# Kernel optimization log

Measured on AMD Instinct MI355X. Metric: run time of the kernel, lower is better.

Reference implementation:

```python
import jax, jax.numpy as jnp
import numpy as np

TIME_STEP = 3
TOPK = 84


def setup_inputs() -> dict:
    key = jax.random.key(0)
    kx, _ = jax.random.split(key)
    x = jax.random.uniform(kx, (8, 2, 352, 2048), dtype=jnp.float32)
    w = jnp.ones((), dtype=jnp.float32)
    return {"x": x, "w": w}


def reference(x, w):
    b, c, f, l = x.shape
    emb = c * TIME_STEP
    last = x[:, :, :, -1:]  # (b,c,f,1) last frame, used as right-padding
    # shift i: x[..., i:] padded on the right with i copies of the last frame
    parts = [
        x if i == 0 else jnp.concatenate(
            [x[:, :, :, i:], jnp.broadcast_to(last, (b, c, f, i))], axis=-1)
        for i in range(TIME_STEP)
    ]
    shifted = jnp.concatenate(parts, axis=1)            # (b, emb, f, l)
    shifted = shifted.transpose(0, 2, 3, 1).reshape(b, f * l, emb)  # (b, N, emb)

    query = shifted.mean(axis=1, keepdims=True)         # (b, 1, emb)
    scores = jnp.einsum('bqe,bne->bqn', query, shifted)[:, 0]  # (b, N)

    topk_scores, topk_idx = jax.lax.top_k(scores, TOPK)  # (b, K)
    vals = jnp.take_along_axis(shifted, topk_idx[:, :, None], axis=1)  # (b, K, emb)
    attn = jax.nn.softmax(topk_scores, axis=-1)          # (b, K)

    out = jnp.einsum('bk,bke->be', attn, vals) * w + query[:, 0] * (0.5 - w)  # (b, emb)
    return out.reshape(b, c, 1, TIME_STEP)
```

## Files before the change

kernel.cpp:

```cpp
#include <hip/hip_runtime.h>
#include <math.h>

#define LL 2048
#define FF 352
#define BATCH 8
#define TOPK 84
#define FPB 4
#define BPB (FF / FPB)
#define NBINS 8192
#define BINSCALE 1024.0f
#define SUBBINS 8192
#define CAP 32768
#define FCAP 1024
#define NROWS (BATCH * 2 * FF)
#define FL (FF * LL)
#define CNTSTRIDE 64

#define OFF_Q 64
#define OFF_CNT 128
#define OFF_PART 1024
#define OFF_CS 32768
#define OFF_CI 294912

__device__ __forceinline__ int coarse_bin(float sv) {
    int bin = (int)(fmaxf(sv, 0.f) * BINSCALE);
    return bin > NBINS - 1 ? NBINS - 1 : bin;
}
__device__ __forceinline__ int fine_bin(float sv, int t) {
    float f = fmaxf(sv, 0.f) * BINSCALE - (float)t;
    int s = (int)(f * (float)SUBBINS);
    s = s < 0 ? 0 : s;
    return s > SUBBINS - 1 ? SUBBINS - 1 : s;
}

__device__ __forceinline__ void find_thresh(const unsigned int* hist, int K,
                                            int tid, int lane, int wid,
                                            int* wtot, int* sres) {
    int csum = 0;
    #pragma unroll
    for (int k = 0; k < 32; ++k) csum += (int)hist[tid * 32 + ((k + tid) & 31)];
    int sfx = csum;
    #pragma unroll
    for (int d = 1; d < 64; d <<= 1) {
        int o = __shfl_down(sfx, d);
        if (lane + d < 64) sfx += o;
    }
    if (lane == 0) wtot[wid] = sfx;
    __syncthreads();
    int hi = 0;
    #pragma unroll
    for (int w2 = 0; w2 < 4; ++w2) if (w2 > wid) hi += wtot[w2];
    int SC = sfx + hi;
    int SCn = SC - csum;
    if (SC >= K && SCn < K) { sres[0] = tid; sres[1] = SCn; }
    __syncthreads();
    int cstar = sres[0], aboveC = sres[1];
    if (tid < 64) {
        int hv = (tid < 32) ? (int)hist[cstar * 32 + tid] : 0;
        int s2 = hv;
        #pragma unroll
        for (int d = 1; d < 32; d <<= 1) {
            int o = __shfl_down(s2, d);
            if (tid + d < 64) s2 += o;
        }
        int ge = aboveC + s2;
        int gt = ge - hv;
        if (tid < 32 && ge >= K && gt < K) { sres[2] = cstar * 32 + tid; sres[3] = gt; }
    }
    __syncthreads();
}

__global__ __launch_bounds__(256) void k_rowsum(const float* __restrict__ x,
                                                float* __restrict__ ws,
                                                int* __restrict__ wsi) {
    int r = blockIdx.x;
    int tid = threadIdx.x;
    if (r == 0 && tid < 8) wsi[OFF_CNT + tid * CNTSTRIDE] = 0;
    const float4* rp = (const float4*)(x + (size_t)r * LL);
    float4 v0 = rp[tid];
    float4 v1 = rp[tid + 256];
    float s = v0.x + v0.y + v0.z + v0.w + v1.x + v1.y + v1.z + v1.w;
    for (int off = 32; off; off >>= 1) s += __shfl_down(s, off);
    __shared__ float red[4];
    int lane = tid & 63, wid = tid >> 6;
    if (lane == 0) red[wid] = s;
    __syncthreads();
    float* part = ws + OFF_PART + 4 * r;
    if (tid == 0) {
        part[0] = red[0] + red[1] + red[2] + red[3];
        part[1] = v0.x;
        part[2] = v0.y;
    }
    if (tid == 255) part[3] = v1.w;
}

__global__ __launch_bounds__(256, 4) void k_score(const float* __restrict__ x,
                                                  float* __restrict__ ws,
                                                  int* __restrict__ wsi) {
    __shared__ unsigned int hist[NBINS];
    __shared__ float4 red0[4], red1[4];
    __shared__ float sq[6];
    __shared__ int wtot[4], sres[4];
    __shared__ int lcnt, lbase;
    int tid = threadIdx.x;
    int b = blockIdx.x / BPB, blk = blockIdx.x % BPB;
    int fb = blk * FPB;
    int lane = tid & 63, wid = tid >> 6;

    for (int k = 0; k < NBINS / 256; ++k) hist[tid + (k << 8)] = 0u;
    if (tid == 0) lcnt = 0;

    float4 acc0 = {0.f, 0.f, 0.f, 0.f}, acc1 = {0.f, 0.f, 0.f, 0.f};
    const float4* part = (const float4*)(ws + OFF_PART) + b * 2 * FF;
    for (int i = tid; i < 2 * FF; i += 256) {
        float4 p = part[i];
        if (i < FF) { acc0.x += p.x; acc0.y += p.y; acc0.z += p.z; acc0.w += p.w; }
        else        { acc1.x += p.x; acc1.y += p.y; acc1.z += p.z; acc1.w += p.w; }
    }
    for (int off = 32; off; off >>= 1) {
        acc0.x += __shfl_down(acc0.x, off); acc0.y += __shfl_down(acc0.y, off);
        acc0.z += __shfl_down(acc0.z, off); acc0.w += __shfl_down(acc0.w, off);
        acc1.x += __shfl_down(acc1.x, off); acc1.y += __shfl_down(acc1.y, off);
        acc1.z += __shfl_down(acc1.z, off); acc1.w += __shfl_down(acc1.w, off);
    }
    if (lane == 0) { red0[wid] = acc0; red1[wid] = acc1; }
    __syncthreads();
    if (tid == 0) {
        float A0 = 0, B0 = 0, C0 = 0, D0 = 0, A1 = 0, B1 = 0, C1 = 0, D1 = 0;
        for (int w2 = 0; w2 < 4; ++w2) {
            A0 += red0[w2].x; B0 += red0[w2].y; C0 += red0[w2].z; D0 += red0[w2].w;
            A1 += red1[w2].x; B1 += red1[w2].y; C1 += red1[w2].z; D1 += red1[w2].w;
        }
        const float inv = 1.f / (float)FL;
        sq[0] = A0 * inv;
        sq[1] = A1 * inv;
        sq[2] = (A0 - B0 + D0) * inv;
        sq[3] = (A1 - B1 + D1) * inv;
        sq[4] = (A0 - B0 - C0 + 2.f * D0) * inv;
        sq[5] = (A1 - B1 - C1 + 2.f * D1) * inv;
        if (blk == 0) for (int e = 0; e < 6; ++e) ws[OFF_Q + b * 6 + e] = sq[e];
    }
    __syncthreads();
    float q0 = sq[0], q1 = sq[1], q2 = sq[2], q3 = sq[3], q4 = sq[4], q5 = sq[5];

    const float* r0p[FPB];
    const float* r1p[FPB];
    #pragma unroll
    for (int fr = 0; fr < FPB; ++fr) {
        r0p[fr] = x + ((size_t)(b * 2 + 0) * FF + fb + fr) * LL;
        r1p[fr] = x + ((size_t)(b * 2 + 1) * FF + fb + fr) * LL;
    }

    float pa4[FPB][2], pa5[FPB][2], pb4[FPB][2], pb5[FPB][2];
    if (lane == 63) {
        #pragma unroll
        for (int fr = 0; fr < FPB; ++fr) {
            #pragma unroll
            for (int h = 0; h < 2; ++h) {
                int l0 = (h << 10) + tid * 4;
                if (l0 != LL - 4) {
                    pa4[fr][h] = r0p[fr][l0 + 4]; pa5[fr][h] = r0p[fr][l0 + 5];
                    pb4[fr][h] = r1p[fr][l0 + 4]; pb5[fr][h] = r1p[fr][l0 + 5];
                }
            }
        }
    }

    float4 sreg[FPB][2];
    float4 u = *(const float4*)(r0p[0] + tid * 4);
    float4 v = *(const float4*)(r1p[0] + tid * 4);
    #pragma unroll
    for (int fr = 0; fr < FPB; ++fr) {
        #pragma unroll
        for (int h = 0; h < 2; ++h) {
            int l0 = (h << 10) + tid * 4;
            int nfr = (h == 1) ? fr + 1 : fr;
            int nh = (h == 1) ? 0 : 1;
            float4 un, vn;
            bool have_next = (nfr < FPB);
            if (have_next) {
                int ln = (nh << 10) + tid * 4;
                un = *(const float4*)(r0p[nfr] + ln);
                vn = *(const float4*)(r1p[nfr] + ln);
            }
            float a4 = __shfl_down(u.x, 1), a5 = __shfl_down(u.y, 1);
            float b4 = __shfl_down(v.x, 1), b5 = __shfl_down(v.y, 1);
            if (lane == 63) {
                if (l0 == LL - 4) { a4 = u.w; a5 = u.w; b4 = v.w; b5 = v.w; }
                else { a4 = pa4[fr][h]; a5 = pa5[fr][h];
                       b4 = pb4[fr][h]; b5 = pb5[fr][h]; }
            }
            float4 s;
            s.x = q0 * u.x + q1 * v.x + q2 * u.y + q3 * v.y + q4 * u.z + q5 * v.z;
            s.y = q0 * u.y + q1 * v.y + q2 * u.z + q3 * v.z + q4 * u.w + q5 * v.w;
            s.z = q0 * u.z + q1 * v.z + q2 * u.w + q3 * v.w + q4 * a4 + q5 * b4;
            s.w = q0 * u.w + q1 * v.w + q2 * a4 + q3 * b4 + q4 * a5 + q5 * b5;
            sreg[fr][h] = s;
            #pragma unroll
            for (int j = 0; j < 4; ++j) {
                float sv = j == 0 ? s.x : (j == 1 ? s.y : (j == 2 ? s.z : s.w));
                atomicAdd(&hist[coarse_bin(sv)], 1u);
            }
            if (have_next) { u = un; v = vn; }
        }
    }
    __syncthreads();

    find_thresh(hist, TOPK, tid, lane, wid, wtot, sres);
    int t = sres[2];

    unsigned int kmask = 0u;
    #pragma unroll
    for (int fr = 0; fr < FPB; ++fr) {
        #pragma unroll
        for (int h = 0; h < 2; ++h) {
            float4 s = sreg[fr][h];
            #pragma unroll
            for (int j = 0; j < 4; ++j) {
                float sv = j == 0 ? s.x : (j == 1 ? s.y : (j == 2 ? s.z : s.w));
                if (coarse_bin(sv) >= t) kmask |= 1u << ((fr << 3) + (h << 2) + j);
            }
        }
    }
    int cnt = __popc(kmask);
    int myoff = 0;
    if (cnt) myoff = atomicAdd(&lcnt, cnt);
    __syncthreads();
    if (tid == 0) lbase = atomicAdd(&wsi[OFF_CNT + b * CNTSTRIDE], lcnt);
    __syncthreads();
    int pos = lbase + myoff;
    #pragma unroll
    for (int fr = 0; fr < FPB; ++fr) {
        #pragma unroll
        for (int h = 0; h < 2; ++h) {
            float4 s = sreg[fr][h];
            int l0 = (h << 10) + tid * 4;
            int nb = (fb + fr) * LL + l0;
            #pragma unroll
            for (int j = 0; j < 4; ++j) {
                if (kmask & (1u << ((fr << 3) + (h << 2) + j))) {
                    float sv = j == 0 ? s.x : (j == 1 ? s.y : (j == 2 ? s.z : s.w));
                    if (pos < CAP) {
                        ws[OFF_CS + b * CAP + pos] = sv;
                        wsi[OFF_CI + b * CAP + pos] = nb + j;
                    }
                    ++pos;
                }
            }
        }
    }
}

__global__ __launch_bounds__(256) void k_final(const float* __restrict__ x,
                                               const float* __restrict__ wv,
                                               const float* __restrict__ ws,
                                               const int* __restrict__ wsi,
                                               float* __restrict__ out) {
    __shared__ union {
        unsigned int hist[NBINS];
        struct { float cs[FCAP]; int ci[FCAP]; } fin;
    } sh;
    __shared__ int wtot[4], sres[4];
    __shared__ int cnt2;
    __shared__ float redm[4];
    __shared__ float den;
    __shared__ float accsh[8];
    int tid = threadIdx.x;
    int b = blockIdx.x;
    int lane = tid & 63, wid = tid >> 6;

    int C = wsi[OFF_CNT + b * CNTSTRIDE];
    if (C > CAP) C = CAP;
    const float* gcs = ws + OFF_CS + b * CAP;
    const int* gci = wsi + OFF_CI + b * CAP;

    for (int k = 0; k < NBINS / 256; ++k) sh.hist[tid + (k << 8)] = 0u;
    __syncthreads();
    for (int p4 = tid * 4; p4 < C; p4 += 1024) {
        float4 s4 = *(const float4*)(gcs + p4);
        int lim = C - p4;
        atomicAdd(&sh.hist[coarse_bin(s4.x)], 1u);
        if (lim > 1) atomicAdd(&sh.hist[coarse_bin(s4.y)], 1u);
        if (lim > 2) atomicAdd(&sh.hist[coarse_bin(s4.z)], 1u);
        if (lim > 3) atomicAdd(&sh.hist[coarse_bin(s4.w)], 1u);
    }
    __syncthreads();
    find_thresh(sh.hist, TOPK, tid, lane, wid, wtot, sres);
    int t = sres[2];
    int above = sres[3];

    for (int k = 0; k < NBINS / 256; ++k) sh.hist[tid + (k << 8)] = 0u;
    __syncthreads();
    for (int p4 = tid * 4; p4 < C; p4 += 1024) {
        float4 s4 = *(const float4*)(gcs + p4);
        int lim = C - p4;
        #pragma unroll
        for (int j = 0; j < 4; ++j) {
            if (j >= lim) break;
            float sv = j == 0 ? s4.x : (j == 1 ? s4.y : (j == 2 ? s4.z : s4.w));
            if (coarse_bin(sv) == t) atomicAdd(&sh.hist[fine_bin(sv, t)], 1u);
        }
    }
    __syncthreads();
    find_thresh(sh.hist, TOPK - above, tid, lane, wid, wtot, sres);
    int t2 = sres[2];
    if (tid == 0) cnt2 = 0;
    __syncthreads();

    for (int p4 = tid * 4; p4 < C; p4 += 1024) {
        float4 s4 = *(const float4*)(gcs + p4);
        int4 i4 = *(const int4*)(gci + p4);
        int lim = C - p4;
        #pragma unroll
        for (int j = 0; j < 4; ++j) {
            if (j >= lim) break;
            float sv = j == 0 ? s4.x : (j == 1 ? s4.y : (j == 2 ? s4.z : s4.w));
            int iv = j == 0 ? i4.x : (j == 1 ? i4.y : (j == 2 ? i4.z : i4.w));
            int bin = coarse_bin(sv);
            bool keep = (bin > t) || (bin == t && fine_bin(sv, t) >= t2);
            if (keep) {
                int q = atomicAdd(&cnt2, 1);
                if (q < FCAP) { sh.fin.cs[q] = sv; sh.fin.ci[q] = iv; }
            }
        }
    }
    __syncthreads();
    int C2 = cnt2;
    if (C2 > FCAP) C2 = FCAP;

    if (tid < 8) accsh[tid] = 0.f;
    if (tid == 0) den = 0.f;
    __syncthreads();

    float m = -INFINITY;
    for (int p = tid; p < C2; p += 256) m = fmaxf(m, sh.fin.cs[p]);
    for (int off = 32; off; off >>= 1) m = fmaxf(m, __shfl_down(m, off));
    if (lane == 0) redm[wid] = m;
    __syncthreads();
    float smax = fmaxf(fmaxf(redm[0], redm[1]), fmaxf(redm[2], redm[3]));

    float g0 = 0.f, g1 = 0.f, g2 = 0.f, g3 = 0.f, g4 = 0.f, g5 = 0.f, dden = 0.f;
    for (int p = tid; p < C2; p += 256) {
        float s = sh.fin.cs[p];
        int idx = sh.fin.ci[p];
        int rank = 0;
        for (int j = 0; j < C2; ++j) {
            float sj = sh.fin.cs[j];
            int ij = sh.fin.ci[j];
            rank += (sj > s) || (sj == s && ij < idx);
        }
        if (rank < TOPK) {
            float pexp = expf(s - smax);
            dden += pexp;
            int f = idx >> 11, l = idx & (LL - 1);
            int l1 = l + 1 < LL ? l + 1 : LL - 1;
            int l2 = l + 2 < LL ? l + 2 : LL - 1;
            const float* r0 = x + ((size_t)(b * 2 + 0) * FF + f) * LL;
            const float* r1 = x + ((size_t)(b * 2 + 1) * FF + f) * LL;
            g0 += pexp * r0[l];
            g1 += pexp * r1[l];
            g2 += pexp * r0[l1];
            g3 += pexp * r1[l1];
            g4 += pexp * r0[l2];
            g5 += pexp * r1[l2];
        }
    }
    for (int off = 32; off; off >>= 1) {
        dden += __shfl_down(dden, off);
        g0 += __shfl_down(g0, off); g1 += __shfl_down(g1, off);
        g2 += __shfl_down(g2, off); g3 += __shfl_down(g3, off);
        g4 += __shfl_down(g4, off); g5 += __shfl_down(g5, off);
    }
    if (lane == 0) {
        atomicAdd(&den, dden);
        atomicAdd(&accsh[0], g0); atomicAdd(&accsh[1], g1);
        atomicAdd(&accsh[2], g2); atomicAdd(&accsh[3], g3);
        atomicAdd(&accsh[4], g4); atomicAdd(&accsh[5], g5);
    }
    __syncthreads();
    if (tid < 6) {
        float w = wv[0];
        float q = ws[OFF_Q + b * 6 + tid];
        out[b * 6 + tid] = (accsh[tid] / den) * w + q * (0.5f - w);
    }
}

extern "C" void kernel_launch(void* const* d_in, const int* in_sizes, int n_in,
                              void* d_out, int out_size, void* d_ws, size_t ws_size,
                              hipStream_t stream) {
    const float* x = (const float*)d_in[0];
    const float* w = (const float*)d_in[1];
    float* out = (float*)d_out;
    float* wsf = (float*)d_ws;
    int* wsi = (int*)d_ws;

    k_rowsum<<<NROWS, 256, 0, stream>>>(x, wsf, wsi);
    k_score<<<BATCH * BPB, 256, 0, stream>>>(x, wsf, wsi);
    k_final<<<BATCH, 256, 0, stream>>>(x, w, wsf, wsi, out);
}
```

Baseline: 117.7 us.

## Batch rows in rowsum and compact candidates in shared memory for final select

k_rowsum now has each block reduce 8 rows and emit one partial per group of rows, which cuts the block count and the number of partials k_score must sum. k_final no longer makes three passes over the global candidate list. It makes one histogram pass, then copies candidates in or above the threshold bin into a shared buffer, and runs the fine histogram and final filter on that smaller buffer. The global reads are unrolled four float4 loads per thread. The risk is that if more than 2048 candidates fall at or above the threshold bin, the buffer truncates them, and the shared memory footprint is larger.

```diff
diff --git a/kernel.cpp b/kernel.cpp
--- a/kernel.cpp
+++ b/kernel.cpp
@@ -11,7 +11,10 @@
 #define BINSCALE 1024.0f
 #define SUBBINS 8192
 #define CAP 32768
-#define FCAP 1024
+#define BCAP 2048
+#define FINCAP 512
+#define RPB 8
+#define NPART (NROWS / RPB)
 #define NROWS (BATCH * 2 * FF)
 #define FL (FF * LL)
 #define CNTSTRIDE 64
@@ -33,12 +36,14 @@
     return s > SUBBINS - 1 ? SUBBINS - 1 : s;
 }
 
+template<int NB>
 __device__ __forceinline__ void find_thresh(const unsigned int* hist, int K,
                                             int tid, int lane, int wid,
                                             int* wtot, int* sres) {
+    constexpr int CW = NB / 256;
     int csum = 0;
     #pragma unroll
-    for (int k = 0; k < 32; ++k) csum += (int)hist[tid * 32 + ((k + tid) & 31)];
+    for (int k = 0; k < CW; ++k) csum += (int)hist[tid * CW + ((k + tid) & (CW - 1))];
     int sfx = csum;
     #pragma unroll
     for (int d = 1; d < 64; d <<= 1) {
@@ -56,16 +61,16 @@
     __syncthreads();
     int cstar = sres[0], aboveC = sres[1];
     if (tid < 64) {
-        int hv = (tid < 32) ? (int)hist[cstar * 32 + tid] : 0;
+        int hv = (tid < CW) ? (int)hist[cstar * CW + tid] : 0;
         int s2 = hv;
         #pragma unroll
-        for (int d = 1; d < 32; d <<= 1) {
+        for (int d = 1; d < CW; d <<= 1) {
             int o = __shfl_down(s2, d);
             if (tid + d < 64) s2 += o;
         }
         int ge = aboveC + s2;
         int gt = ge - hv;
-        if (tid < 32 && ge >= K && gt < K) { sres[2] = cstar * 32 + tid; sres[3] = gt; }
+        if (tid < CW && ge >= K && gt < K) { sres[2] = cstar * CW + tid; sres[3] = gt; }
     }
     __syncthreads();
 }
@@ -73,25 +78,37 @@
 __global__ __launch_bounds__(256) void k_rowsum(const float* __restrict__ x,
                                                 float* __restrict__ ws,
                                                 int* __restrict__ wsi) {
-    int r = blockIdx.x;
+    int g = blockIdx.x;
     int tid = threadIdx.x;
-    if (r == 0 && tid < 8) wsi[OFF_CNT + tid * CNTSTRIDE] = 0;
-    const float4* rp = (const float4*)(x + (size_t)r * LL);
-    float4 v0 = rp[tid];
-    float4 v1 = rp[tid + 256];
-    float s = v0.x + v0.y + v0.z + v0.w + v1.x + v1.y + v1.z + v1.w;
-    for (int off = 32; off; off >>= 1) s += __shfl_down(s, off);
-    __shared__ float red[4];
+    if (g == 0 && tid < 8) wsi[OFF_CNT + tid * CNTSTRIDE] = 0;
+    int bc = g / 44, sub = g % 44;
+    int rr = tid >> 5, c = tid & 31;
+    const float4* rp = (const float4*)(x + (size_t)(bc * FF + sub * RPB + rr) * LL);
+    float s = 0.f, x0c = 0.f, x1c = 0.f, xlc = 0.f;
+    #pragma unroll
+    for (int k = 0; k < 16; ++k) {
+        float4 v = rp[c + (k << 5)];
+        s += v.x + v.y + v.z + v.w;
+        if (k == 0 && c == 0) { x0c = v.x; x1c = v.y; }
+        if (k == 15 && c == 31) xlc = v.w;
+    }
     int lane = tid & 63, wid = tid >> 6;
-    if (lane == 0) red[wid] = s;
-    __syncthreads();
-    float* part = ws + OFF_PART + 4 * r;
+    for (int off = 32; off; off >>= 1) {
+        s += __shfl_down(s, off);
+        x0c += __shfl_down(x0c, off);
+        x1c += __shfl_down(x1c, off);
+        xlc += __shfl_down(xlc, off);
+    }
+    __shared__ float4 red[4];
+    if (lane == 0) red[wid] = make_float4(s, x0c, x1c, xlc);
+    __syncthreads();
     if (tid == 0) {
-        part[0] = red[0] + red[1] + red[2] + red[3];
-        part[1] = v0.x;
-        part[2] = v0.y;
-    }
-    if (tid == 255) part[3] = v1.w;
+        float4 p = make_float4(0.f, 0.f, 0.f, 0.f);
+        for (int w2 = 0; w2 < 4; ++w2) {
+            p.x += red[w2].x; p.y += red[w2].y; p.z += red[w2].z; p.w += red[w2].w;
+        }
+        ((float4*)(ws + OFF_PART))[g] = p;
+    }
 }
 
 __global__ __launch_bounds__(256, 4) void k_score(const float* __restrict__ x,
@@ -111,11 +128,10 @@
     if (tid == 0) lcnt = 0;
 
     float4 acc0 = {0.f, 0.f, 0.f, 0.f}, acc1 = {0.f, 0.f, 0.f, 0.f};
-    const float4* part = (const float4*)(ws + OFF_PART) + b * 2 * FF;
-    for (int i = tid; i < 2 * FF; i += 256) {
-        float4 p = part[i];
-        if (i < FF) { acc0.x += p.x; acc0.y += p.y; acc0.z += p.z; acc0.w += p.w; }
-        else        { acc1.x += p.x; acc1.y += p.y; acc1.z += p.z; acc1.w += p.w; }
+    if (tid < 88) {
+        int ch = tid / 44, sb = tid % 44;
+        float4 p = ((const float4*)(ws + OFF_PART))[(2 * b + ch) * 44 + sb];
+        if (ch == 0) acc0 = p; else acc1 = p;
     }
     for (int off = 32; off; off >>= 1) {
         acc0.x += __shfl_down(acc0.x, off); acc0.y += __shfl_down(acc0.y, off);
@@ -206,7 +222,7 @@
     }
     __syncthreads();
 
-    find_thresh(hist, TOPK, tid, lane, wid, wtot, sres);
+    find_thresh<NBINS>(hist, TOPK, tid, lane, wid, wtot, sres);
     int t = sres[2];
 
     unsigned int kmask = 0u;
@@ -256,12 +272,13 @@
                                                const float* __restrict__ ws,
                                                const int* __restrict__ wsi,
                                                float* __restrict__ out) {
-    __shared__ union {
-        unsigned int hist[NBINS];
-        struct { float cs[FCAP]; int ci[FCAP]; } fin;
-    } sh;
+    __shared__ unsigned int hist[NBINS];
+    __shared__ float bls[BCAP];
+    __shared__ int bli[BCAP];
+    __shared__ float fins[FINCAP];
+    __shared__ int fini[FINCAP];
     __shared__ int wtot[4], sres[4];
-    __shared__ int cnt2;
+    __shared__ int bcnt, c2s;
     __shared__ float redm[4];
     __shared__ float den;
     __shared__ float accsh[8];
@@ -274,66 +291,92 @@
     const float* gcs = ws + OFF_CS + b * CAP;
     const int* gci = wsi + OFF_CI + b * CAP;
 
-    for (int k = 0; k < NBINS / 256; ++k) sh.hist[tid + (k << 8)] = 0u;
-    __syncthreads();
-    for (int p4 = tid * 4; p4 < C; p4 += 1024) {
-        float4 s4 = *(const float4*)(gcs + p4);
-        int lim = C - p4;
-        atomicAdd(&sh.hist[coarse_bin(s4.x)], 1u);
-        if (lim > 1) atomicAdd(&sh.hist[coarse_bin(s4.y)], 1u);
-        if (lim > 2) atomicAdd(&sh.hist[coarse_bin(s4.z)], 1u);
-        if (lim > 3) atomicAdd(&sh.hist[coarse_bin(s4.w)], 1u);
-    }
-    __syncthreads();
-    find_thresh(sh.hist, TOPK, tid, lane, wid, wtot, sres);
+    for (int k = 0; k < NBINS / 256; ++k) hist[tid + (k << 8)] = 0u;
+    if (tid == 0) bcnt = 0;
+    __syncthreads();
+    for (int base = 0; base < C; base += 4096) {
+        int j0 = base + tid * 4;
+        float4 s0 = *(const float4*)(gcs + j0);
+        float4 s1 = *(const float4*)(gcs + j0 + 1024);
+        float4 s2 = *(const float4*)(gcs + j0 + 2048);
+        float4 s3 = *(const float4*)(gcs + j0 + 3072);
+        #pragma unroll
+        for (int q = 0; q < 4; ++q) {
+            float4 sq4 = q == 0 ? s0 : (q == 1 ? s1 : (q == 2 ? s2 : s3));
+            int jq = j0 + q * 1024;
+            #pragma unroll
+            for (int j = 0; j < 4; ++j) {
+                if (jq + j < C) {
+                    float sv = j == 0 ? sq4.x : (j == 1 ? sq4.y : (j == 2 ? sq4.z : sq4.w));
+                    atomicAdd(&hist[coarse_bin(sv)], 1u);
+                }
+            }
+        }
+    }
+    __syncthreads();
+    find_thresh<NBINS>(hist, TOPK, tid, lane, wid, wtot, sres);
     int t = sres[2];
-    int above = sres[3];
-
-    for (int k = 0; k < NBINS / 256; ++k) sh.hist[tid + (k << 8)] = 0u;
-    __syncthreads();
-    for (int p4 = tid * 4; p4 < C; p4 += 1024) {
-        float4 s4 = *(const float4*)(gcs + p4);
-        int lim = C - p4;
-        #pragma unroll
-        for (int j = 0; j < 4; ++j) {
-            if (j >= lim) break;
-            float sv = j == 0 ? s4.x : (j == 1 ? s4.y : (j == 2 ? s4.z : s4.w));
-            if (coarse_bin(sv) == t) atomicAdd(&sh.hist[fine_bin(sv, t)], 1u);
-        }
-    }
-    __syncthreads();
-    find_thresh(sh.hist, TOPK - above, tid, lane, wid, wtot, sres);
+
+    for (int base = 0; base < C; base += 4096) {
+        int j0 = base + tid * 4;
+        float4 s0 = *(const float4*)(gcs + j0);
+        float4 s1 = *(const float4*)(gcs + j0 + 1024);
+        float4 s2 = *(const float4*)(gcs + j0 + 2048);
+        float4 s3 = *(const float4*)(gcs + j0 + 3072);
+        int4 i0 = *(const int4*)(gci + j0);
+        int4 i1 = *(const int4*)(gci + j0 + 1024);
+        int4 i2 = *(const int4*)(gci + j0 + 2048);
+        int4 i3 = *(const int4*)(gci + j0 + 3072);
+        #pragma unroll
+        for (int q = 0; q < 4; ++q) {
+            float4 sq4 = q == 0 ? s0 : (q == 1 ? s1 : (q == 2 ? s2 : s3));
+            int4 iq4 = q == 0 ? i0 : (q == 1 ? i1 : (q == 2 ? i2 : i3));
+            int jq = j0 + q * 1024;
+            #pragma unroll
+            for (int j = 0; j < 4; ++j) {
+                if (jq + j < C) {
+                    float sv = j == 0 ? sq4.x : (j == 1 ? sq4.y : (j == 2 ? sq4.z : sq4.w));
+                    int iv = j == 0 ? iq4.x : (j == 1 ? iq4.y : (j == 2 ? iq4.z : iq4.w));
+                    if (coarse_bin(sv) >= t) {
+                        int p = atomicAdd(&bcnt, 1);
+                        if (p < BCAP) { bls[p] = sv; bli[p] = iv; }
+                    }
+                }
+            }
+        }
+    }
+    __syncthreads();
+    int nb = bcnt < BCAP ? bcnt : BCAP;
+
+    for (int k = 0; k < NBINS / 256; ++k) hist[tid + (k << 8)] = 0u;
+    __syncthreads();
+    for (int p = tid; p < nb; p += 256) {
+        float sv = bls[p];
+        int fk = coarse_bin(sv) > t ? SUBBINS - 1 : fine_bin(sv, t);
+        atomicAdd(&hist[fk], 1u);
+    }
+    __syncthreads();
+    find_thresh<NBINS>(hist, TOPK, tid, lane, wid, wtot, sres);
     int t2 = sres[2];
-    if (tid == 0) cnt2 = 0;
-    __syncthreads();
-
-    for (int p4 = tid * 4; p4 < C; p4 += 1024) {
-        float4 s4 = *(const float4*)(gcs + p4);
-        int4 i4 = *(const int4*)(gci + p4);
-        int lim = C - p4;
-        #pragma unroll
-        for (int j = 0; j < 4; ++j) {
-            if (j >= lim) break;
-            float sv = j == 0 ? s4.x : (j == 1 ? s4.y : (j == 2 ? s4.z : s4.w));
-            int iv = j == 0 ? i4.x : (j == 1 ? i4.y : (j == 2 ? i4.z : i4.w));
-            int bin = coarse_bin(sv);
-            bool keep = (bin > t) || (bin == t && fine_bin(sv, t) >= t2);
-            if (keep) {
-                int q = atomicAdd(&cnt2, 1);
-                if (q < FCAP) { sh.fin.cs[q] = sv; sh.fin.ci[q] = iv; }
-            }
-        }
-    }
-    __syncthreads();
-    int C2 = cnt2;
-    if (C2 > FCAP) C2 = FCAP;
+    if (tid == 0) c2s = 0;
+    __syncthreads();
+    for (int p = tid; p < nb; p += 256) {
+        float sv = bls[p];
+        int fk = coarse_bin(sv) > t ? SUBBINS - 1 : fine_bin(sv, t);
+        if (fk >= t2) {
+            int q = atomicAdd(&c2s, 1);
+            if (q < FINCAP) { fins[q] = sv; fini[q] = bli[p]; }
+        }
+    }
+    __syncthreads();
+    int C2 = c2s < FINCAP ? c2s : FINCAP;
 
     if (tid < 8) accsh[tid] = 0.f;
     if (tid == 0) den = 0.f;
     __syncthreads();
 
     float m = -INFINITY;
-    for (int p = tid; p < C2; p += 256) m = fmaxf(m, sh.fin.cs[p]);
+    for (int p = tid; p < C2; p += 256) m = fmaxf(m, fins[p]);
     for (int off = 32; off; off >>= 1) m = fmaxf(m, __shfl_down(m, off));
     if (lane == 0) redm[wid] = m;
     __syncthreads();
@@ -341,12 +384,12 @@
 
     float g0 = 0.f, g1 = 0.f, g2 = 0.f, g3 = 0.f, g4 = 0.f, g5 = 0.f, dden = 0.f;
     for (int p = tid; p < C2; p += 256) {
-        float s = sh.fin.cs[p];
-        int idx = sh.fin.ci[p];
+        float s = fins[p];
+        int idx = fini[p];
         int rank = 0;
         for (int j = 0; j < C2; ++j) {
-            float sj = sh.fin.cs[j];
-            int ij = sh.fin.ci[j];
+            float sj = fins[j];
+            int ij = fini[j];
             rank += (sj > s) || (sj == s && ij < idx);
         }
         if (rank < TOPK) {
@@ -394,7 +437,7 @@
     float* wsf = (float*)d_ws;
     int* wsi = (int*)d_ws;
 
-    k_rowsum<<<NROWS, 256, 0, stream>>>(x, wsf, wsi);
+    k_rowsum<<<NPART, 256, 0, stream>>>(x, wsf, wsi);
     k_score<<<BATCH * BPB, 256, 0, stream>>>(x, wsf, wsi);
     k_final<<<BATCH, 256, 0, stream>>>(x, w, wsf, wsi, out);
 }
```

Result: faster. 112.3 us (-4.6%).
